# Kernel tuning notes

Measured on AMD Instinct MI355X. Metric: run time of the kernel, lower is better.

The kernel has to match this reference:

```python
import jax, jax.numpy as jnp
import numpy as np

B, T, C = 2, 2048, 1024
H = 16
HS = C // H  # 64
FF = 4 * C


def setup_inputs() -> dict:
    key = jax.random.key(0)
    ks = jax.random.split(key, 8)
    s = 0.02
    x = jax.random.normal(ks[0], (B, T, C), dtype=jnp.float32)
    # per-head projection weights, stacked: y = einsum('btc,hcd->bhtd', x, W)
    Wq = jax.random.normal(ks[1], (H, C, HS), dtype=jnp.float32) * s
    Wk = jax.random.normal(ks[2], (H, C, HS), dtype=jnp.float32) * s
    Wv = jax.random.normal(ks[3], (H, C, HS), dtype=jnp.float32) * s
    # nn.Linear weight layout: [out, in]
    Wproj = jax.random.normal(ks[4], (C, H * HS), dtype=jnp.float32) * s
    W1 = jax.random.normal(ks[5], (FF, C), dtype=jnp.float32) * s
    b1 = jnp.zeros((FF,), dtype=jnp.float32)
    W2 = jax.random.normal(ks[6], (C, FF), dtype=jnp.float32) * s
    return {"x": x, "Wq": Wq, "Wk": Wk, "Wv": Wv, "Wproj": Wproj,
            "W1": W1, "b1": b1, "W2": W2}


def reference(x, Wq, Wk, Wv, Wproj, W1, b1, W2):
    Bb, Tt, Cc = x.shape
    # --- multi-head causal self-attention ---
    q = jnp.einsum('btc,hcd->bhtd', x, Wq)
    k = jnp.einsum('btc,hcd->bhtd', x, Wk)
    v = jnp.einsum('btc,hcd->bhtd', x, Wv)
    scale = HS ** (-0.5)
    scores = jnp.einsum('bhtd,bhsd->bhts', q, k) * scale  # [B,H,T,T]
    causal_mask = jnp.triu(jnp.ones((Tt, Tt), dtype=bool), k=1)
    scores = jnp.where(causal_mask, -jnp.inf, scores)
    wei = jax.nn.softmax(scores, axis=-1)
    attn = jnp.einsum('bhts,bhsd->bhtd', wei, v)  # [B,H,T,HS]
    attn = attn.transpose(0, 2, 1, 3).reshape(Bb, Tt, H * HS)  # concat heads
    sa = attn @ Wproj.T  # [B,T,C]
    x = x + sa
    # --- SiLU MLP ---
    h = jax.nn.silu(x @ W1.T + b1)
    x = x + h @ W2.T
    return x
```

## Files before the change

kernel.cpp:

```cpp
#include <hip/hip_runtime.h>

#define BB 2
#define TT 2048
#define CC 1024
#define HH 16
#define HS 64
#define FF 4096
#define MTOK 4096

typedef __attribute__((ext_vector_type(4))) float f32x4;
typedef __attribute__((ext_vector_type(8))) short short8;

__device__ __forceinline__ unsigned short f2b(float f) {
  unsigned int u = __builtin_bit_cast(unsigned int, f);
  u += 0x7fffu + ((u >> 16) & 1u);
  return (unsigned short)(u >> 16);
}

__device__ __forceinline__ float fast_exp2(float x) {
#if __has_builtin(__builtin_amdgcn_exp2f)
  return __builtin_amdgcn_exp2f(x);
#else
  return exp2f(x);
#endif
}

__device__ __forceinline__ unsigned int cvt_pk_bf16(float lo, float hi) {
  unsigned int r;
  asm("v_cvt_pk_bf16_f32 %0, %1, %2" : "=v"(r) : "v"(lo), "v"(hi));
  return r;
}

__global__ void cast_bf16_kernel(const float* __restrict__ src,
                                 unsigned short* __restrict__ dst, int n8) {
  int i = blockIdx.x * 256 + threadIdx.x;
  if (i >= n8) return;
  f32x4 a = reinterpret_cast<const f32x4*>(src)[2 * i];
  f32x4 b = reinterpret_cast<const f32x4*>(src)[2 * i + 1];
  short8 o;
  o[0] = (short)f2b(a[0]); o[1] = (short)f2b(a[1]);
  o[2] = (short)f2b(a[2]); o[3] = (short)f2b(a[3]);
  o[4] = (short)f2b(b[0]); o[5] = (short)f2b(b[1]);
  o[6] = (short)f2b(b[2]); o[7] = (short)f2b(b[3]);
  reinterpret_cast<short8*>(dst)[i] = o;
}

__global__ void prep_wqkv_kernel(const float* __restrict__ wq,
                                 const float* __restrict__ wk,
                                 const float* __restrict__ wv,
                                 unsigned short* __restrict__ dst) {
  __shared__ float tile[64][65];
  const int qkv = blockIdx.y >> 4;
  const int h = blockIdx.y & 15;
  const int c0 = blockIdx.x * 64;
  const float* w = (qkv == 0) ? wq : (qkv == 1) ? wk : wv;
  const float scale = (qkv == 0) ? 0.125f : 1.0f;
  const int dd = threadIdx.x & 63;
  const int rr = threadIdx.x >> 6;
  const float* src = w + ((size_t)h * 1024 + c0) * 64;
#pragma unroll
  for (int it = 0; it < 16; ++it) {
    int c = it * 4 + rr;
    tile[c][dd] = src[(size_t)c * 64 + dd];
  }
  __syncthreads();
  unsigned short* dbase = dst + ((size_t)(qkv * 1024 + h * 64)) * 1024 + c0;
#pragma unroll
  for (int it = 0; it < 16; ++it) {
    int d = it * 4 + rr;
    dbase[(size_t)d * 1024 + dd] = f2b(tile[dd][d] * scale);
  }
}

template <int EPI>
__global__ __launch_bounds__(256) void gemm_bt(
    const unsigned short* __restrict__ A, const unsigned short* __restrict__ Bt,
    const int K, const int N, const float* __restrict__ bias,
    const float* __restrict__ resid, float* __restrict__ outf,
    unsigned short* __restrict__ outb, unsigned short* __restrict__ qout,
    unsigned short* __restrict__ kout, unsigned short* __restrict__ vout) {
  __shared__ __align__(16) unsigned short ldsA[3][128 * 64];
  __shared__ __align__(16) unsigned short ldsB[3][128 * 64];
  const int tid = threadIdx.x;
  const int lane = tid & 63;
  const int wave = tid >> 6;
  const int g = lane >> 4, l16 = lane & 15;
  const int wr = wave >> 1, wc = wave & 1;

  const int gx = gridDim.x;
  const int nwg = gx * gridDim.y;
  const int lid = blockIdx.y * gx + blockIdx.x;
  const int qch = nwg >> 3;
  const int swz = (lid & 7) * qch + (lid >> 3);
  const int bm = swz / gx;
  const int bn = swz % gx;

  const int srow = lane >> 3;
  const int schunk = (lane & 7) ^ srow;

  f32x4 acc[4][4] = {};

  const size_t a_row0 = (size_t)bm * 128;
  const size_t b_row0 = (size_t)bn * 128;

  auto STAGE = [&](int step, int buf) {
    const int kt = step * 64;
#pragma unroll
    for (int i = 0; i < 4; ++i) {
      const int row = (wave * 4 + i) * 8 + srow;
      const unsigned short* ga = A + (a_row0 + row) * K + kt + schunk * 8;
      __builtin_amdgcn_global_load_lds(
          (const __attribute__((address_space(1))) unsigned int*)ga,
          (__attribute__((address_space(3))) unsigned int*)(ldsA[buf] + (wave * 4 + i) * 512),
          16, 0, 0);
      const unsigned short* gb = Bt + (b_row0 + row) * K + kt + schunk * 8;
      __builtin_amdgcn_global_load_lds(
          (const __attribute__((address_space(1))) unsigned int*)gb,
          (__attribute__((address_space(3))) unsigned int*)(ldsB[buf] + (wave * 4 + i) * 512),
          16, 0, 0);
    }
  };

  const int nsteps = K >> 6;
  STAGE(0, 0);
  STAGE(1, 1);
  int buf = 0;
  for (int t = 0; t < nsteps; ++t) {
    if (t < nsteps - 1) {
      asm volatile("s_waitcnt vmcnt(8)" ::: "memory");
    } else {
      asm volatile("s_waitcnt vmcnt(0)" ::: "memory");
    }
    __builtin_amdgcn_s_barrier();
    asm volatile("" ::: "memory");
    const unsigned short* bA = ldsA[buf];
    const unsigned short* bB = ldsB[buf];
    short8 af[4][2], bfr[4][2];
#pragma unroll
    for (int mi = 0; mi < 4; ++mi)
#pragma unroll
      for (int ks = 0; ks < 2; ++ks) {
        int row = wr * 64 + mi * 16 + l16;
        int ch = (ks * 4 + g) ^ (row & 7);
        af[mi][ks] = *reinterpret_cast<const short8*>(&bA[row * 64 + ch * 8]);
      }
#pragma unroll
    for (int ni = 0; ni < 4; ++ni)
#pragma unroll
      for (int ks = 0; ks < 2; ++ks) {
        int row = wc * 64 + ni * 16 + l16;
        int ch = (ks * 4 + g) ^ (row & 7);
        bfr[ni][ks] = *reinterpret_cast<const short8*>(&bB[row * 64 + ch * 8]);
      }
    if (t + 2 < nsteps) {
      int nb = buf + 2;
      if (nb >= 3) nb -= 3;
      STAGE(t + 2, nb);
    }
    __builtin_amdgcn_s_setprio(1);
#pragma unroll
    for (int ks = 0; ks < 2; ++ks)
#pragma unroll
      for (int mi = 0; mi < 4; ++mi)
#pragma unroll
        for (int ni = 0; ni < 4; ++ni)
          acc[mi][ni] = __builtin_amdgcn_mfma_f32_16x16x32_bf16(
              af[mi][ks], bfr[ni][ks], acc[mi][ni], 0, 0, 0);
    __builtin_amdgcn_s_setprio(0);
    buf = (buf == 2) ? 0 : buf + 1;
  }

#pragma unroll
  for (int mi = 0; mi < 4; ++mi) {
#pragma unroll
    for (int ni = 0; ni < 4; ++ni) {
#pragma unroll
      for (int j = 0; j < 4; ++j) {
        const int row = bm * 128 + wr * 64 + mi * 16 + g * 4 + j;
        const int col = bn * 128 + wc * 64 + ni * 16 + l16;
        float v = acc[mi][ni][j];
        if (EPI == 0) {
          int qkv = col >> 10;
          int hd = col & 1023;
          int h = hd >> 6, d = hd & 63;
          int b = row >> 11, t = row & 2047;
          size_t base = (size_t)(b * HH + h) * (TT * HS);
          if (qkv == 0) {
            qout[base + ((size_t)t << 6) + d] = f2b(v);
          } else if (qkv == 1) {
            size_t off = ((size_t)((t >> 4) * 2 + (d >> 5)) << 9) +
                         ((((d >> 3) & 3) * 16 + (t & 15)) << 3) + (d & 7);
            kout[base + off] = f2b(v);
          } else {
            size_t off = ((size_t)((t >> 6) * 8 + ((d >> 4) << 1) + ((t & 63) >> 5)) << 9) +
                         ((((t >> 3) & 3) * 16 + (d & 15)) << 3) + (t & 7);
            vout[base + off] = f2b(v);
          }
        } else if (EPI == 1) {
          size_t idx = (size_t)row * N + col;
          float r = resid[idx] + v;
          outf[idx] = r;
          outb[idx] = f2b(r);
        } else if (EPI == 2) {
          float pre = v + bias[col];
          float sg = 1.0f / (1.0f + __expf(-pre));
          outb[(size_t)row * N + col] = f2b(pre * sg);
        } else {
          size_t idx = (size_t)row * N + col;
          outf[idx] += v;
        }
      }
    }
  }
}

#define PSTRIDE 66
__global__ __launch_bounds__(256, 4) void attn_fwd(
    const unsigned short* __restrict__ qg, const unsigned short* __restrict__ kg,
    const unsigned short* __restrict__ vtg, unsigned short* __restrict__ att) {
  __shared__ __align__(16) unsigned short plds[4][16 * PSTRIDE];
  __shared__ float olds[4][16][65];
  __shared__ float mlds[4][16], llds[4][16];
  const int lane = threadIdx.x & 63;
  const int wave = threadIdx.x >> 6;
  const int g = lane >> 4, l16 = lane & 15;
  const int bid = blockIdx.x;
  const int bh = (bid & 7) * 4 + ((bid >> 3) & 3);
  const int b = bh >> 4, h = bh & 15;
  const int pi = wave >> 1, split = wave & 1;
  const int pr = (bid >> 5) * 2 + pi;
  const unsigned short* qh = qg + (size_t)bh * (TT * HS);
  const unsigned short* kh = kg + (size_t)bh * (TT * HS);
  const unsigned short* vth = vtg + (size_t)bh * (TT * HS);
  unsigned short* pw = plds[wave];
  const float L2E = 1.4426950408889634f;

  for (int half = 0; half < 2; ++half) {
    const int tile = half ? (127 - pr) : pr;
    const int r0 = tile * 16;

    short8 qf[2];
#pragma unroll
    for (int ks = 0; ks < 2; ++ks)
      qf[ks] = *reinterpret_cast<const short8*>(
          qh + (size_t)(r0 + l16) * 64 + ks * 32 + g * 8);

    f32x4 oacc[4] = {};
    float mrow = -1e30f, lrow = 0.f;

    const int nkt = (r0 + 79) >> 6;
    for (int kt = split; kt < nkt; kt += 2) {
      const int s0 = kt << 6;
      short8 kf[4][2];
#pragma unroll
      for (int ni = 0; ni < 4; ++ni)
#pragma unroll
        for (int ks = 0; ks < 2; ++ks)
          kf[ni][ks] = *reinterpret_cast<const short8*>(
              kh + (((size_t)(kt * 4 + ni) * 2 + ks) << 9) + lane * 8);
      f32x4 s[4] = {};
      __builtin_amdgcn_s_setprio(1);
#pragma unroll
      for (int ks = 0; ks < 2; ++ks)
#pragma unroll
        for (int ni = 0; ni < 4; ++ni)
          s[ni] = __builtin_amdgcn_mfma_f32_16x16x32_bf16(kf[ni][ks], qf[ks],
                                                          s[ni], 0, 0, 0);
      __builtin_amdgcn_s_setprio(0);
      short8 vf[4][2];
#pragma unroll
      for (int dn = 0; dn < 4; ++dn)
#pragma unroll
        for (int ks = 0; ks < 2; ++ks)
          vf[dn][ks] = *reinterpret_cast<const short8*>(
              vth + (((size_t)(kt * 8 + dn * 2 + ks)) << 9) + lane * 8);
      if (kt == nkt - 1) {
        const int sq = r0 + l16;
#pragma unroll
        for (int ni = 0; ni < 4; ++ni)
#pragma unroll
          for (int j = 0; j < 4; ++j) {
            int sk = s0 + ni * 16 + g * 4 + j;
            if (sk > sq) s[ni][j] = -1e30f;
          }
      }
      float t0 = fmaxf(fmaxf(s[0][0], s[0][1]), fmaxf(s[0][2], s[0][3]));
      float t1 = fmaxf(fmaxf(s[1][0], s[1][1]), fmaxf(s[1][2], s[1][3]));
      float t2 = fmaxf(fmaxf(s[2][0], s[2][1]), fmaxf(s[2][2], s[2][3]));
      float t3 = fmaxf(fmaxf(s[3][0], s[3][1]), fmaxf(s[3][2], s[3][3]));
      float cm = fmaxf(fmaxf(t0, t1), fmaxf(t2, t3));
      cm = fmaxf(cm, __shfl_xor(cm, 16));
      cm = fmaxf(cm, __shfl_xor(cm, 32));
      if (__any(cm > mrow + 8.0f)) {
        float mnew = fmaxf(mrow, cm);
        float sc = fast_exp2((mrow - mnew) * L2E);
        mrow = mnew;
        lrow *= sc;
#pragma unroll
        for (int j = 0; j < 4; ++j) {
          float scj = __shfl(sc, g * 4 + j);
#pragma unroll
          for (int dn = 0; dn < 4; ++dn) oacc[dn][j] *= scj;
        }
      }
      const float mL = mrow * L2E;
#pragma unroll
      for (int ni = 0; ni < 4; ++ni)
#pragma unroll
        for (int j = 0; j < 4; ++j)
          s[ni][j] = fast_exp2(__builtin_fmaf(s[ni][j], L2E, -mL));
      float a0 = (s[0][0] + s[0][1]) + (s[0][2] + s[0][3]);
      float a1 = (s[1][0] + s[1][1]) + (s[1][2] + s[1][3]);
      float a2 = (s[2][0] + s[2][1]) + (s[2][2] + s[2][3]);
      float a3 = (s[3][0] + s[3][1]) + (s[3][2] + s[3][3]);
      float ps = (a0 + a1) + (a2 + a3);
      ps += __shfl_xor(ps, 16);
      ps += __shfl_xor(ps, 32);
      lrow += ps;
#pragma unroll
      for (int ni = 0; ni < 4; ++ni) {
        unsigned int w0 = cvt_pk_bf16(s[ni][0], s[ni][1]);
        unsigned int w1 = cvt_pk_bf16(s[ni][2], s[ni][3]);
        unsigned int* pd =
            reinterpret_cast<unsigned int*>(&pw[l16 * PSTRIDE + ni * 16 + g * 4]);
        pd[0] = w0;
        pd[1] = w1;
      }
      asm volatile("" ::: "memory");
      short8 pa[2];
#pragma unroll
      for (int ks = 0; ks < 2; ++ks)
        pa[ks] = *reinterpret_cast<const short8*>(&pw[l16 * PSTRIDE + ks * 32 + g * 8]);
      __builtin_amdgcn_s_setprio(1);
#pragma unroll
      for (int ks = 0; ks < 2; ++ks)
#pragma unroll
        for (int dn = 0; dn < 4; ++dn)
          oacc[dn] = __builtin_amdgcn_mfma_f32_16x16x32_bf16(pa[ks], vf[dn][ks],
                                                             oacc[dn], 0, 0, 0);
      __builtin_amdgcn_s_setprio(0);
      asm volatile("" ::: "memory");
    }
#pragma unroll
    for (int dn = 0; dn < 4; ++dn)
#pragma unroll
      for (int j = 0; j < 4; ++j)
        olds[wave][g * 4 + j][dn * 16 + l16] = oacc[dn][j];
    if (lane < 16) {
      mlds[wave][lane] = mrow;
      llds[wave][lane] = lrow;
    }
    __syncthreads();
    if (split == 0) {
#pragma unroll
      for (int j = 0; j < 4; ++j) {
        const int q = g * 4 + j;
        float mA = mlds[wave][q], lA = llds[wave][q];
        float mB = mlds[wave ^ 1][q], lB = llds[wave ^ 1][q];
        float ms = fmaxf(mA, mB);
        float a = fast_exp2((mA - ms) * L2E);
        float bb = fast_exp2((mB - ms) * L2E);
        float rinv = 1.0f / (lA * a + lB * bb);
        int t = r0 + q;
#pragma unroll
        for (int dn = 0; dn < 4; ++dn) {
          float ob = olds[wave ^ 1][q][dn * 16 + l16];
          float val = (oacc[dn][j] * a + ob * bb) * rinv;
          att[((size_t)(b * TT + t)) * CC + h * 64 + dn * 16 + l16] = f2b(val);
        }
      }
    }
    __syncthreads();
  }
}

extern "C" void kernel_launch(void* const* d_in, const int* in_sizes, int n_in,
                              void* d_out, int out_size, void* d_ws, size_t ws_size,
                              hipStream_t stream) {
  const float* x = (const float*)d_in[0];
  const float* Wq = (const float*)d_in[1];
  const float* Wk = (const float*)d_in[2];
  const float* Wv = (const float*)d_in[3];
  const float* Wproj = (const float*)d_in[4];
  const float* W1 = (const float*)d_in[5];
  const float* b1 = (const float*)d_in[6];
  const float* W2 = (const float*)d_in[7];
  float* out = (float*)d_out;
  char* ws = (char*)d_ws;
  const size_t MB = 1024 * 1024;
  unsigned short* xb = (unsigned short*)(ws + 0 * MB);
  unsigned short* wqkvT = (unsigned short*)(ws + 8 * MB);
  unsigned short* wprojb = (unsigned short*)(ws + 14 * MB);
  unsigned short* w1b = (unsigned short*)(ws + 16 * MB);
  unsigned short* w2b = (unsigned short*)(ws + 24 * MB);
  unsigned short* qb = (unsigned short*)(ws + 32 * MB);
  unsigned short* kpk = (unsigned short*)(ws + 40 * MB);
  unsigned short* vpk = (unsigned short*)(ws + 48 * MB);
  unsigned short* att = (unsigned short*)(ws + 64 * MB);
  unsigned short* x1b = (unsigned short*)(ws + 72 * MB);
  unsigned short* hb = (unsigned short*)(ws + 80 * MB);

  cast_bf16_kernel<<<2048, 256, 0, stream>>>(x, xb, 4194304 / 8);
  cast_bf16_kernel<<<512, 256, 0, stream>>>(Wproj, wprojb, 1048576 / 8);
  cast_bf16_kernel<<<2048, 256, 0, stream>>>(W1, w1b, 4194304 / 8);
  cast_bf16_kernel<<<2048, 256, 0, stream>>>(W2, w2b, 4194304 / 8);
  prep_wqkv_kernel<<<dim3(16, 48), 256, 0, stream>>>(Wq, Wk, Wv, wqkvT);

  gemm_bt<0><<<dim3(24, 32), 256, 0, stream>>>(xb, wqkvT, 1024, 3072, nullptr,
                                               nullptr, nullptr, nullptr, qb, kpk, vpk);
  attn_fwd<<<1024, 256, 0, stream>>>(qb, kpk, vpk, att);
  gemm_bt<1><<<dim3(8, 32), 256, 0, stream>>>(att, wprojb, 1024, 1024, nullptr,
                                              x, out, x1b, nullptr, nullptr, nullptr);
  gemm_bt<2><<<dim3(32, 32), 256, 0, stream>>>(x1b, w1b, 1024, 4096, b1, nullptr,
                                               nullptr, hb, nullptr, nullptr, nullptr);
  gemm_bt<3><<<dim3(8, 32), 256, 0, stream>>>(hb, w2b, 4096, 1024, nullptr, nullptr,
                                              out, nullptr, nullptr, nullptr, nullptr);
  (void)in_sizes; (void)n_in; (void)out_size; (void)ws_size;
}
```

Measured before the change: 241.4 us.

## Use eight waves per GEMM tile and merge four cast launches into one

```diff
diff --git a/kernel.cpp b/kernel.cpp
--- a/kernel.cpp
+++ b/kernel.cpp
@@ -31,18 +31,37 @@
   return r;
 }
 
-__global__ void cast_bf16_kernel(const float* __restrict__ src,
-                                 unsigned short* __restrict__ dst, int n8) {
+__global__ void cast_all_kernel(const float* __restrict__ x,
+                                const float* __restrict__ wp,
+                                const float* __restrict__ w1,
+                                const float* __restrict__ w2,
+                                unsigned short* __restrict__ xb,
+                                unsigned short* __restrict__ wpb,
+                                unsigned short* __restrict__ w1b,
+                                unsigned short* __restrict__ w2b) {
   int i = blockIdx.x * 256 + threadIdx.x;
-  if (i >= n8) return;
-  f32x4 a = reinterpret_cast<const f32x4*>(src)[2 * i];
-  f32x4 b = reinterpret_cast<const f32x4*>(src)[2 * i + 1];
+  const float* src;
+  unsigned short* dst;
+  int off;
+  if (i < 524288) {
+    src = x; dst = xb; off = i;
+  } else if (i < 655360) {
+    src = wp; dst = wpb; off = i - 524288;
+  } else if (i < 1179648) {
+    src = w1; dst = w1b; off = i - 655360;
+  } else if (i < 1703936) {
+    src = w2; dst = w2b; off = i - 1179648;
+  } else {
+    return;
+  }
+  f32x4 a = reinterpret_cast<const f32x4*>(src)[2 * off];
+  f32x4 b = reinterpret_cast<const f32x4*>(src)[2 * off + 1];
   short8 o;
   o[0] = (short)f2b(a[0]); o[1] = (short)f2b(a[1]);
   o[2] = (short)f2b(a[2]); o[3] = (short)f2b(a[3]);
   o[4] = (short)f2b(b[0]); o[5] = (short)f2b(b[1]);
   o[6] = (short)f2b(b[2]); o[7] = (short)f2b(b[3]);
-  reinterpret_cast<short8*>(dst)[i] = o;
+  reinterpret_cast<short8*>(dst)[off] = o;
 }
 
 __global__ void prep_wqkv_kernel(const float* __restrict__ wq,
@@ -73,7 +92,7 @@
 }
 
 template <int EPI>
-__global__ __launch_bounds__(256) void gemm_bt(
+__global__ __launch_bounds__(512) void gemm_bt(
     const unsigned short* __restrict__ A, const unsigned short* __restrict__ Bt,
     const int K, const int N, const float* __restrict__ bias,
     const float* __restrict__ resid, float* __restrict__ outf,
@@ -85,7 +104,8 @@
   const int lane = tid & 63;
   const int wave = tid >> 6;
   const int g = lane >> 4, l16 = lane & 15;
-  const int wr = wave >> 1, wc = wave & 1;
+  const int wr = wave >> 2;
+  const int wc = wave & 3;
 
   const int gx = gridDim.x;
   const int nwg = gx * gridDim.y;
@@ -98,7 +118,7 @@
   const int srow = lane >> 3;
   const int schunk = (lane & 7) ^ srow;
 
-  f32x4 acc[4][4] = {};
+  f32x4 acc[4][2] = {};
 
   const size_t a_row0 = (size_t)bm * 128;
   const size_t b_row0 = (size_t)bn * 128;
@@ -106,17 +126,17 @@
   auto STAGE = [&](int step, int buf) {
     const int kt = step * 64;
 #pragma unroll
-    for (int i = 0; i < 4; ++i) {
-      const int row = (wave * 4 + i) * 8 + srow;
+    for (int i = 0; i < 2; ++i) {
+      const int row = (wave * 2 + i) * 8 + srow;
       const unsigned short* ga = A + (a_row0 + row) * K + kt + schunk * 8;
       __builtin_amdgcn_global_load_lds(
           (const __attribute__((address_space(1))) unsigned int*)ga,
-          (__attribute__((address_space(3))) unsigned int*)(ldsA[buf] + (wave * 4 + i) * 512),
+          (__attribute__((address_space(3))) unsigned int*)(ldsA[buf] + (wave * 2 + i) * 512),
           16, 0, 0);
       const unsigned short* gb = Bt + (b_row0 + row) * K + kt + schunk * 8;
       __builtin_amdgcn_global_load_lds(
           (const __attribute__((address_space(1))) unsigned int*)gb,
-          (__attribute__((address_space(3))) unsigned int*)(ldsB[buf] + (wave * 4 + i) * 512),
+          (__attribute__((address_space(3))) unsigned int*)(ldsB[buf] + (wave * 2 + i) * 512),
           16, 0, 0);
     }
   };
@@ -127,7 +147,7 @@
   int buf = 0;
   for (int t = 0; t < nsteps; ++t) {
     if (t < nsteps - 1) {
-      asm volatile("s_waitcnt vmcnt(8)" ::: "memory");
+      asm volatile("s_waitcnt vmcnt(4)" ::: "memory");
     } else {
       asm volatile("s_waitcnt vmcnt(0)" ::: "memory");
     }
@@ -135,7 +155,7 @@
     asm volatile("" ::: "memory");
     const unsigned short* bA = ldsA[buf];
     const unsigned short* bB = ldsB[buf];
-    short8 af[4][2], bfr[4][2];
+    short8 af[4][2], bfr[2][2];
 #pragma unroll
     for (int mi = 0; mi < 4; ++mi)
 #pragma unroll
@@ -145,10 +165,10 @@
         af[mi][ks] = *reinterpret_cast<const short8*>(&bA[row * 64 + ch * 8]);
       }
 #pragma unroll
-    for (int ni = 0; ni < 4; ++ni)
+    for (int ni = 0; ni < 2; ++ni)
 #pragma unroll
       for (int ks = 0; ks < 2; ++ks) {
-        int row = wc * 64 + ni * 16 + l16;
+        int row = wc * 32 + ni * 16 + l16;
         int ch = (ks * 4 + g) ^ (row & 7);
         bfr[ni][ks] = *reinterpret_cast<const short8*>(&bB[row * 64 + ch * 8]);
       }
@@ -163,7 +183,7 @@
 #pragma unroll
       for (int mi = 0; mi < 4; ++mi)
 #pragma unroll
-        for (int ni = 0; ni < 4; ++ni)
+        for (int ni = 0; ni < 2; ++ni)
           acc[mi][ni] = __builtin_amdgcn_mfma_f32_16x16x32_bf16(
               af[mi][ks], bfr[ni][ks], acc[mi][ni], 0, 0, 0);
     __builtin_amdgcn_s_setprio(0);
@@ -173,11 +193,11 @@
 #pragma unroll
   for (int mi = 0; mi < 4; ++mi) {
 #pragma unroll
-    for (int ni = 0; ni < 4; ++ni) {
+    for (int ni = 0; ni < 2; ++ni) {
 #pragma unroll
       for (int j = 0; j < 4; ++j) {
         const int row = bm * 128 + wr * 64 + mi * 16 + g * 4 + j;
-        const int col = bn * 128 + wc * 64 + ni * 16 + l16;
+        const int col = bn * 128 + wc * 32 + ni * 16 + l16;
         float v = acc[mi][ni][j];
         if (EPI == 0) {
           int qkv = col >> 10;
@@ -400,20 +420,17 @@
   unsigned short* x1b = (unsigned short*)(ws + 72 * MB);
   unsigned short* hb = (unsigned short*)(ws + 80 * MB);
 
-  cast_bf16_kernel<<<2048, 256, 0, stream>>>(x, xb, 4194304 / 8);
-  cast_bf16_kernel<<<512, 256, 0, stream>>>(Wproj, wprojb, 1048576 / 8);
-  cast_bf16_kernel<<<2048, 256, 0, stream>>>(W1, w1b, 4194304 / 8);
-  cast_bf16_kernel<<<2048, 256, 0, stream>>>(W2, w2b, 4194304 / 8);
+  cast_all_kernel<<<6656, 256, 0, stream>>>(x, Wproj, W1, W2, xb, wprojb, w1b, w2b);
   prep_wqkv_kernel<<<dim3(16, 48), 256, 0, stream>>>(Wq, Wk, Wv, wqkvT);
 
-  gemm_bt<0><<<dim3(24, 32), 256, 0, stream>>>(xb, wqkvT, 1024, 3072, nullptr,
+  gemm_bt<0><<<dim3(24, 32), 512, 0, stream>>>(xb, wqkvT, 1024, 3072, nullptr,
                                                nullptr, nullptr, nullptr, qb, kpk, vpk);
   attn_fwd<<<1024, 256, 0, stream>>>(qb, kpk, vpk, att);
-  gemm_bt<1><<<dim3(8, 32), 256, 0, stream>>>(att, wprojb, 1024, 1024, nullptr,
+  gemm_bt<1><<<dim3(8, 32), 512, 0, stream>>>(att, wprojb, 1024, 1024, nullptr,
                                               x, out, x1b, nullptr, nullptr, nullptr);
-  gemm_bt<2><<<dim3(32, 32), 256, 0, stream>>>(x1b, w1b, 1024, 4096, b1, nullptr,
+  gemm_bt<2><<<dim3(32, 32), 512, 0, stream>>>(x1b, w1b, 1024, 4096, b1, nullptr,
                                                nullptr, hb, nullptr, nullptr, nullptr);
-  gemm_bt<3><<<dim3(8, 32), 256, 0, stream>>>(hb, w2b, 4096, 1024, nullptr, nullptr,
+  gemm_bt<3><<<dim3(8, 32), 512, 0, stream>>>(hb, w2b, 4096, 1024, nullptr, nullptr,
                                               out, nullptr, nullptr, nullptr, nullptr);
   (void)in_sizes; (void)n_in; (void)out_size; (void)ws_size;
 }
```

After: 215.1 us. 10.9% less time.
